# Kernel tuning notes

Hardware: AMD Instinct MI355X
Metric: run time of the kernel (lower is better)

## Reference

```python
import jax, jax.numpy as jnp
import numpy as np

# Tokenizer hyperparams (match init_kwargs)
NUM_VARS = 8
EMBED = 64
WIN = 16
STEP = 4
SWIDTH = 1.0  # sample_width
PWIDTH = 1.0  # patch_width
BATCH = 32
SAMPLES = 4096


def setup_inputs() -> dict:
    key = jax.random.key(0)
    k1, k2, k3, k4, k5 = jax.random.split(key, 5)
    return {
        "x": jax.random.normal(k1, (BATCH, NUM_VARS, SAMPLES), dtype=jnp.float32),
        "W1": jax.random.normal(k2, (NUM_VARS, EMBED), dtype=jnp.float32),   # sample-level LSH hyperplanes
        "b1": jax.random.normal(k3, (EMBED,), dtype=jnp.float32),
        "W2": jax.random.normal(k4, (WIN * EMBED, EMBED), dtype=jnp.float32),  # patch-level LSH hyperplanes
        "b2": jax.random.normal(k5, (EMBED,), dtype=jnp.float32),
    }


def reference(x, W1, b1, W2, b2):
    B, V, S = x.shape
    # encode(): per-timestep sample-level LSH hash, fully vectorized over S.
    # torch loop does sample_level(x[:,:,ix]) for each ix -> one batched einsum here.
    # e: [B, EMBED, S]
    e = jnp.floor((jnp.einsum('bvs,vd->bds', x, W1) + b1[None, :, None]) / SWIDTH)

    # quantize(): sliding windows over the time axis.
    starts = jnp.arange(0, S - WIN, STEP)                 # [T] window start positions
    idx = starts[:, None] + jnp.arange(WIN)[None, :]
    wins = e[:, :, idx]
    T = starts.shape[0]
    flat = wins.transpose(0, 2, 1, 3).reshape(B, T, EMBED * WIN)
    # patch-level LSH hash per window
    tokens = jnp.floor((jnp.einsum('btf,fe->bte', flat, W2) + b2) / PWIDTH)  # [B, T, EMBED]
    return tokens
```

## Files before the change

kernel.cpp:

```cpp
#include <hip/hip_runtime.h>
#include <cstdint>
#include <cstddef>

#define B_ 32
#define V_ 8
#define S_ 4096
#define E_ 64
#define T_ 1020
#define TT 32
#define SLP 144

typedef __bf16 bf16_t;
typedef bf16_t bf16x8 __attribute__((ext_vector_type(8)));
typedef float f32x4 __attribute__((ext_vector_type(4)));

__global__ __launch_bounds__(256) void prep_kernel(const float* __restrict__ W2,
                                                   bf16_t* __restrict__ w2sw) {
  const int q = blockIdx.x * 256 + threadIdx.x;
  const int l = q & 63, nt = (q >> 6) & 3, kk = q >> 8;
  const int fb = kk * 32 + (l >> 4) * 8;
  const int n = nt * 16 + (l & 15);
  bf16x8 v;
#pragma unroll
  for (int j = 0; j < 8; ++j) v[j] = (bf16_t)W2[(fb + j) * E_ + n];
  *reinterpret_cast<bf16x8*>(w2sw + (size_t)q * 8) = v;
}

__global__ __launch_bounds__(256, 4) void fused_kernel(const float* __restrict__ x,
                                                       const float* __restrict__ W1,
                                                       const float* __restrict__ b1,
                                                       const bf16_t* __restrict__ w2sw,
                                                       const float* __restrict__ b2,
                                                       float* __restrict__ out) {
  __shared__ float w1s[V_ * E_];
  __shared__ float b1s[E_];
  __shared__ bf16_t et[E_ * SLP];
  const int tid = threadIdx.x;
  const int b = blockIdx.y;
  const int t0 = blockIdx.x * TT;
  for (int i = tid; i < V_ * E_; i += 256) w1s[i] = W1[i];
  if (tid < E_) b1s[tid] = b1[tid];
  __syncthreads();
  {
    const int dbase = (tid >> 7) * 32;
    const int sl = tid & 127;
    const int s0 = 4 * t0;
    int s_a = s0 + sl;        if (s_a > S_ - 1) s_a = S_ - 1;
    int s_b = s0 + sl + 128;  if (s_b > S_ - 1) s_b = S_ - 1;
    const bool has2 = (sl + 128) < 140;
    float xv0[V_], xv1[V_];
#pragma unroll
    for (int v = 0; v < V_; ++v) {
      xv0[v] = x[((size_t)(b * V_ + v) << 12) + s_a];
      xv1[v] = x[((size_t)(b * V_ + v) << 12) + s_b];
    }
    for (int d = dbase; d < dbase + 32; ++d) {
      float a0 = b1s[d], a1 = b1s[d];
#pragma unroll
      for (int v = 0; v < V_; ++v) {
        a0 += xv0[v] * w1s[v * E_ + d];
        a1 += xv1[v] * w1s[v * E_ + d];
      }
      et[d * SLP + sl] = (bf16_t)floorf(a0);
      if (has2) et[d * SLP + sl + 128] = (bf16_t)floorf(a1);
    }
  }
  __syncthreads();
  const int lane = tid & 63;
  const int wv = tid >> 6;
  const int l15 = lane & 15;
  const int g = lane >> 4;
  const char* etb = reinterpret_cast<const char*>(et);
  const uint32_t aoff = 288u * (g >> 1) + 8u * l15 + 16u * (g & 1);
  const bf16_t* bptr = w2sw + (((size_t)wv * 64 + lane) << 3);
  const float bv = b2[wv * 16 + l15];
  f32x4 acc0 = {bv, bv, bv, bv};
  f32x4 acc1 = {bv, bv, bv, bv};
#pragma unroll 4
  for (int kk = 0; kk < 32; ++kk) {
    const char* pa = etb + aoff + 576 * kk;
    union { uint64_t q[2]; bf16x8 v; } A0, A1;
    A0.q[0] = *reinterpret_cast<const uint64_t*>(pa);
    A0.q[1] = *reinterpret_cast<const uint64_t*>(pa + 8);
    A1.q[0] = *reinterpret_cast<const uint64_t*>(pa + 128);
    A1.q[1] = *reinterpret_cast<const uint64_t*>(pa + 136);
    const bf16x8 Bf = *reinterpret_cast<const bf16x8*>(bptr + ((size_t)kk << 11));
    acc0 = __builtin_amdgcn_mfma_f32_16x16x32_bf16(A0.v, Bf, acc0, 0, 0, 0);
    acc1 = __builtin_amdgcn_mfma_f32_16x16x32_bf16(A1.v, Bf, acc1, 0, 0, 0);
  }
#pragma unroll
  for (int r = 0; r < 4; ++r) {
    const int t1 = t0 + g * 4 + r;
    if (t1 < T_) out[((size_t)(b * T_ + t1)) * E_ + wv * 16 + l15] = floorf(acc0[r]);
    const int t2 = t0 + 16 + g * 4 + r;
    if (t2 < T_) out[((size_t)(b * T_ + t2)) * E_ + wv * 16 + l15] = floorf(acc1[r]);
  }
}

extern "C" void kernel_launch(void* const* d_in, const int* in_sizes, int n_in,
                              void* d_out, int out_size, void* d_ws, size_t ws_size,
                              hipStream_t stream) {
  const float* x  = (const float*)d_in[0];
  const float* W1 = (const float*)d_in[1];
  const float* b1 = (const float*)d_in[2];
  const float* W2 = (const float*)d_in[3];
  const float* b2 = (const float*)d_in[4];
  float* out = (float*)d_out;

  bf16_t* w2sw = (bf16_t*)d_ws;

  hipLaunchKernelGGL(prep_kernel, dim3(32), dim3(256), 0, stream, W2, w2sw);
  hipLaunchKernelGGL(fused_kernel, dim3((T_ + TT - 1) / TT, B_), dim3(256), 0, stream,
                     x, W1, b1, w2sw, b2, out);
}
```

Measured before the change: 23.04 us.

## Restructure sample-hash stage: register-blocked 8x5 tiles, drop W1 shared staging

```diff
diff --git a/kernel.cpp b/kernel.cpp
--- a/kernel.cpp
+++ b/kernel.cpp
@@ -8,7 +8,7 @@
 #define E_ 64
 #define T_ 1020
 #define TT 32
-#define SLP 144
+#define SLP 200
 
 typedef __bf16 bf16_t;
 typedef bf16_t bf16x8 __attribute__((ext_vector_type(8)));
@@ -32,37 +32,40 @@
                                                        const bf16_t* __restrict__ w2sw,
                                                        const float* __restrict__ b2,
                                                        float* __restrict__ out) {
-  __shared__ float w1s[V_ * E_];
-  __shared__ float b1s[E_];
   __shared__ bf16_t et[E_ * SLP];
   const int tid = threadIdx.x;
   const int b = blockIdx.y;
   const int t0 = blockIdx.x * TT;
-  for (int i = tid; i < V_ * E_; i += 256) w1s[i] = W1[i];
-  if (tid < E_) b1s[tid] = b1[tid];
-  __syncthreads();
   {
-    const int dbase = (tid >> 7) * 32;
-    const int sl = tid & 127;
+    const int dg = tid >> 5;
+    const int sg = tid & 31;
     const int s0 = 4 * t0;
-    int s_a = s0 + sl;        if (s_a > S_ - 1) s_a = S_ - 1;
-    int s_b = s0 + sl + 128;  if (s_b > S_ - 1) s_b = S_ - 1;
-    const bool has2 = (sl + 128) < 140;
-    float xv0[V_], xv1[V_];
+    float xv[V_][5];
 #pragma unroll
     for (int v = 0; v < V_; ++v) {
-      xv0[v] = x[((size_t)(b * V_ + v) << 12) + s_a];
-      xv1[v] = x[((size_t)(b * V_ + v) << 12) + s_b];
+#pragma unroll
+      for (int k = 0; k < 5; ++k) {
+        int s = s0 + sg + 32 * k;
+        if (s > S_ - 1) s = S_ - 1;
+        xv[v][k] = x[((size_t)(b * V_ + v) << 12) + s];
+      }
     }
-    for (int d = dbase; d < dbase + 32; ++d) {
-      float a0 = b1s[d], a1 = b1s[d];
+#pragma unroll
+    for (int dd = 0; dd < 8; ++dd) {
+      const int d = dg * 8 + dd;
+      const float bb = b1[d];
+      float acc[5];
+#pragma unroll
+      for (int k = 0; k < 5; ++k) acc[k] = bb;
 #pragma unroll
       for (int v = 0; v < V_; ++v) {
-        a0 += xv0[v] * w1s[v * E_ + d];
-        a1 += xv1[v] * w1s[v * E_ + d];
+        const float w = W1[v * E_ + d];
+#pragma unroll
+        for (int k = 0; k < 5; ++k) acc[k] += xv[v][k] * w;
       }
-      et[d * SLP + sl] = (bf16_t)floorf(a0);
-      if (has2) et[d * SLP + sl + 128] = (bf16_t)floorf(a1);
+#pragma unroll
+      for (int k = 0; k < 5; ++k)
+        et[d * SLP + sg + 32 * k] = (bf16_t)floorf(acc[k]);
     }
   }
   __syncthreads();
@@ -71,14 +74,14 @@
   const int l15 = lane & 15;
   const int g = lane >> 4;
   const char* etb = reinterpret_cast<const char*>(et);
-  const uint32_t aoff = 288u * (g >> 1) + 8u * l15 + 16u * (g & 1);
+  const uint32_t aoff = 400u * (g >> 1) + 8u * l15 + 16u * (g & 1);
   const bf16_t* bptr = w2sw + (((size_t)wv * 64 + lane) << 3);
   const float bv = b2[wv * 16 + l15];
   f32x4 acc0 = {bv, bv, bv, bv};
   f32x4 acc1 = {bv, bv, bv, bv};
 #pragma unroll 4
   for (int kk = 0; kk < 32; ++kk) {
-    const char* pa = etb + aoff + 576 * kk;
+    const char* pa = etb + aoff + 800 * kk;
     union { uint64_t q[2]; bf16x8 v; } A0, A1;
     A0.q[0] = *reinterpret_cast<const uint64_t*>(pa);
     A0.q[1] = *reinterpret_cast<const uint64_t*>(pa + 8);
```

After: 21.35 us. -7.3%, faster.
